# Optimization experiments

Measured on AMD Instinct MI355X. Metric: run time of the kernel, lower is better.

Reference implementation:

```python
import jax, jax.numpy as jnp
import numpy as np

B = 16          # graphs per batch
NN = 2000       # nodes per graph (num_nodes)
N = B * NN      # total nodes in the batched graph
F_IN = 128      # input node features
H, C = 4, 64    # heads, per-head out channels (both GAT layers)
HC = H * C
DEG = 12        # average degree per node
FC1, FC2, OUT = 512, 128, 1
FC_IN = 6 * NN  # len(which_layer) = 6


def setup_inputs() -> dict:
    key = jax.random.key(0)
    ks = jax.random.split(key, 32)

    def g(i, shape, s=0.05):
        return jax.random.normal(ks[i], shape, jnp.float32) * s

    # within-graph random edges, no self loops (GATConv removes then re-adds them)
    src_l = jax.random.randint(ks[0], (B, NN * DEG), 0, NN)
    off = jax.random.randint(ks[1], (B, NN * DEG), 1, NN)
    dst_l = (src_l + off) % NN
    goff = (jnp.arange(B) * NN)[:, None]
    edge_index = jnp.stack([(src_l + goff).reshape(-1),
                            (dst_l + goff).reshape(-1)]).astype(jnp.int32)

    return {
        "x": g(2, (N, F_IN), 1.0),
        "W1": g(3, (F_IN, HC)), "att_src1": g(4, (H, C)), "att_dst1": g(5, (H, C)),
        "b1": jnp.zeros((HC,), jnp.float32),
        "W2": g(6, (HC, HC)), "att_src2": g(7, (H, C)), "att_dst2": g(8, (H, C)),
        "b2": jnp.zeros((HC,), jnp.float32),
        "pw1": g(9, (HC, 1)), "pb1": jnp.zeros((1,), jnp.float32),
        "pw2": g(10, (HC, 1)), "pb2": jnp.zeros((1,), jnp.float32),
        "ln_w": jnp.ones((NN,), jnp.float32), "ln_b": jnp.zeros((NN,), jnp.float32),
        "sex_emb": g(11, (2, NN)), "mut_emb": g(12, (4, NN)),
        "age_w": g(13, (NN,)), "age_b": jnp.zeros((NN,), jnp.float32),
        "fw1": g(14, (FC_IN, FC1)), "fb1": jnp.zeros((FC1,), jnp.float32),
        "fw2": g(15, (FC1, FC2)), "fb2": jnp.zeros((FC2,), jnp.float32),
        "fw3": g(16, (FC2, OUT)), "fb3": jnp.zeros((OUT,), jnp.float32),
        "age": jax.random.uniform(ks[17], (B,), jnp.float32),
        "edge_index": edge_index,
        "sex": jax.random.randint(ks[18], (B,), 0, 2),
        "mutation": jax.random.randint(ks[19], (B,), 0, 4),
    }


def _layer_norm(x, w, b, eps=1e-5):
    mu = jnp.mean(x, -1, keepdims=True)
    var = jnp.mean((x - mu) ** 2, -1, keepdims=True)
    return (x - mu) / jnp.sqrt(var + eps) * w + b


def _gat_conv(x, W, att_src, att_dst, bias, src, dst):
    h = (x @ W).reshape(N, H, C)                         # [N,H,C]
    a_s = jnp.sum(h * att_src[None], -1)                 # [N,H]
    a_d = jnp.sum(h * att_dst[None], -1)                 # [N,H]
    alpha = jax.nn.leaky_relu(a_s[src] + a_d[dst], 0.2)  # [E,H]
    m = jax.ops.segment_max(alpha, dst, num_segments=N)  # segment softmax over dst
    e = jnp.exp(alpha - m[dst])
    denom = jax.ops.segment_sum(e, dst, num_segments=N)
    a = e / (denom[dst] + 1e-16)
    out = jax.ops.segment_sum(a[:, :, None] * h[src], dst, num_segments=N)
    return out.reshape(N, HC) + bias


def _forward(x, W1, att_src1, att_dst1, b1, W2, att_src2, att_dst2, b2,
             pw1, pb1, pw2, pb2, ln_w, ln_b, sex_emb, mut_emb, age_w, age_b,
             fw1, fb1, fw2, fb2, fw3, fb3, age, edge_index, sex, mutation):
    loop = jnp.arange(N, dtype=edge_index.dtype)         # self loops added by GATConv
    src = jnp.concatenate([edge_index[0], loop])
    dst = jnp.concatenate([edge_index[1], loop])

    x0 = jnp.mean(x, -1).reshape(B, NN)                  # to_dense_batch(mean(x,-1))

    h = jax.nn.relu(_gat_conv(x, W1, att_src1, att_dst1, b1, src, dst))
    x1 = (h @ pw1 + pb1).squeeze(-1).reshape(B, NN)
    h = jax.nn.relu(_gat_conv(h, W2, att_src2, att_dst2, b2, src, dst))
    x2 = (h @ pw2 + pb2).squeeze(-1).reshape(B, NN)

    x0 = _layer_norm(x0, ln_w, ln_b)
    x1 = _layer_norm(x1, ln_w, ln_b)
    x2 = _layer_norm(x2, ln_w, ln_b)
    ms = jnp.concatenate([x0, x1, x2], axis=1)           # [B, 3*NN]

    demo = jnp.concatenate([sex_emb[sex], mut_emb[mutation],
                            age[:, None] * age_w[None, :] + age_b], axis=1)
    t = jnp.concatenate([demo, ms], axis=1)              # [B, 6*NN]
    t = jax.nn.relu(t @ fw1 + fb1)
    t = jax.nn.relu(t @ fw2 + fb2)
    pred = t @ fw3 + fb3                                 # [B, 1]
    return pred, x0, x1, x2, ms


def reference(x, W1, att_src1, att_dst1, b1, W2, att_src2, att_dst2, b2,
              pw1, pb1, pw2, pb2, ln_w, ln_b, sex_emb, mut_emb, age_w, age_b,
              fw1, fb1, fw2, fb2, fw3, fb3, age, edge_index, sex, mutation):
    return _forward(x, W1, att_src1, att_dst1, b1, W2, att_src2, att_dst2, b2,
                    pw1, pb1, pw2, pb2, ln_w, ln_b, sex_emb, mut_emb, age_w, age_b,
                    fw1, fb1, fw2, fb2, fw3, fb3, age, edge_index, sex, mutation)
```

## Files before the change

### kernel.cpp

```cpp
#include <hip/hip_runtime.h>
#include <math.h>

#define NTOT   32000
#define NNODE  2000
#define NB     16
#define FIN    128
#define HCDIM  256
#define NH     4
#define FC1DIM 512
#define FC2DIM 128
#define FCIN   12000
#define KC1    50
#define NCH1   240
#define CAP    64
#define BK     32
#define LPITCH 40
#define TRB    384
#define DEMOB  375

typedef __attribute__((ext_vector_type(8))) short bf16x8;
typedef __attribute__((ext_vector_type(4))) float f32x4;

__device__ inline float4 ld4(const float* p){ return *reinterpret_cast<const float4*>(p); }
__device__ inline void st4(float* p, float4 v){ *reinterpret_cast<float4*>(p) = v; }
__device__ inline float4 add4(float4 a, float4 b){ return make_float4(a.x+b.x,a.y+b.y,a.z+b.z,a.w+b.w); }
__device__ inline float lrelu(float x){ return x > 0.f ? x : 0.2f*x; }
__device__ inline float4 leaky4(float4 a){ return make_float4(lrelu(a.x),lrelu(a.y),lrelu(a.z),lrelu(a.w)); }
__device__ inline float4 exp4u(float4 a){ return make_float4(__expf(a.x),__expf(a.y),__expf(a.z),__expf(a.w)); }
__device__ inline float dot4(float4 a, float4 b){ return a.x*b.x + a.y*b.y + a.z*b.z + a.w*b.w; }
__device__ inline float selh(float4 v, int h){ return h==0 ? v.x : (h==1 ? v.y : (h==2 ? v.z : v.w)); }

__device__ inline unsigned short f2bf(float f){
  unsigned int u = __float_as_uint(f);
  u += 0x7FFFu + ((u >> 16) & 1u);
  return (unsigned short)(u >> 16);
}
__device__ inline float bf2f(unsigned short h){
  return __uint_as_float(((unsigned int)h) << 16);
}
__device__ inline float4 ldbf4(const unsigned short* p){
  ushort4 v = *reinterpret_cast<const ushort4*>(p);
  return make_float4(bf2f(v.x), bf2f(v.y), bf2f(v.z), bf2f(v.w));
}

__global__ __launch_bounds__(256) void k_prep(const float* __restrict__ x,
                                              unsigned short* __restrict__ xb,
                                              float* __restrict__ x0r,
                                              int* __restrict__ cnt){
  int gid = blockIdx.x*256 + threadIdx.x;
  if(gid < NTOT) cnt[gid] = 0;
  int lane = threadIdx.x & 63, wv = threadIdx.x >> 6;
  int n = blockIdx.x*4 + wv;
  const float* r = x + (size_t)n*FIN;
  float2 v = *reinterpret_cast<const float2*>(r + lane*2);
  unsigned int packed = (unsigned int)f2bf(v.x) | ((unsigned int)f2bf(v.y) << 16);
  *reinterpret_cast<unsigned int*>(xb + (size_t)n*FIN + lane*2) = packed;
  float s = v.x + v.y;
  #pragma unroll
  for(int off=1; off<64; off<<=1) s += __shfl_xor(s, off);
  if(lane == 0) x0r[n] = s * (1.0f/FIN);
}

__global__ void k_misc(const int* __restrict__ src, const int* __restrict__ dst,
                       int* __restrict__ cnt, int* __restrict__ col, int e0, int eb,
                       const float* __restrict__ W1, const float* __restrict__ W2,
                       unsigned short* __restrict__ W1t, unsigned short* __restrict__ W2t,
                       const float* __restrict__ sexemb, const float* __restrict__ mutemb,
                       const float* __restrict__ agew, const float* __restrict__ ageb,
                       const float* __restrict__ age, const int* __restrict__ sex,
                       const int* __restrict__ mut, float* __restrict__ t){
  int blk = blockIdx.x;
  if(blk < eb){
    int i = blk*256 + threadIdx.x;
    if(i < e0){
      int d = dst[i];
      int slot = atomicAdd(&cnt[d], 1);
      if(slot < CAP) col[(d<<6) + slot] = src[i];
    }
  } else if(blk < eb + TRB){
    int idx = (blk - eb)*256 + threadIdx.x;
    if(idx < HCDIM*FIN){
      int n = idx / FIN, k = idx - n*FIN;
      W1t[idx] = f2bf(W1[(size_t)k*HCDIM + n]);
    } else {
      int j = idx - HCDIM*FIN;
      int n = j / HCDIM, k = j - n*HCDIM;
      W2t[j] = f2bf(W2[(size_t)k*HCDIM + n]);
    }
  } else {
    int i = (blk - eb - TRB)*256 + threadIdx.x;
    int b = i / (3*NNODE);
    int j = i - b*(3*NNODE);
    float v;
    if(j < NNODE)          v = sexemb[sex[b]*NNODE + j];
    else if(j < 2*NNODE)   v = mutemb[mut[b]*NNODE + (j - NNODE)];
    else                   v = age[b]*agew[j - 2*NNODE] + ageb[j - 2*NNODE];
    t[b*FCIN + j] = v;
  }
}

__global__ __launch_bounds__(256) void k_gemm_bf(const unsigned short* __restrict__ A,
                                                 const unsigned short* __restrict__ Bt,
                                                 unsigned short* __restrict__ C,
                                                 const float* __restrict__ attS,
                                                 const float* __restrict__ attD,
                                                 float* __restrict__ a_s,
                                                 float* __restrict__ a_d,
                                                 int M, int K){
  __shared__ unsigned short As[128][LPITCH];
  __shared__ unsigned short Bs[128][LPITCH];
  int tid = threadIdx.x;
  int lane = tid & 63, wv = tid >> 6;
  int wm = (wv & 1)*64, wn = (wv >> 1)*64;
  int m0 = blockIdx.y*128, n0 = blockIdx.x*128;
  int l15 = lane & 15, lq = lane >> 4;
  f32x4 acc[4][4];
  #pragma unroll
  for(int i=0;i<4;i++)
    #pragma unroll
    for(int j=0;j<4;j++)
      acc[i][j] = (f32x4){0.f,0.f,0.f,0.f};

  int r = tid >> 2, c = (tid & 3)*8;
  for(int k0 = 0; k0 < K; k0 += BK){
    *reinterpret_cast<uint4*>(&As[r][c])    = *reinterpret_cast<const uint4*>(A  + (size_t)(m0+r)*K + k0 + c);
    *reinterpret_cast<uint4*>(&As[r+64][c]) = *reinterpret_cast<const uint4*>(A  + (size_t)(m0+r+64)*K + k0 + c);
    *reinterpret_cast<uint4*>(&Bs[r][c])    = *reinterpret_cast<const uint4*>(Bt + (size_t)(n0+r)*K + k0 + c);
    *reinterpret_cast<uint4*>(&Bs[r+64][c]) = *reinterpret_cast<const uint4*>(Bt + (size_t)(n0+r+64)*K + k0 + c);
    __syncthreads();
    bf16x8 af[4], bfr[4];
    #pragma unroll
    for(int i=0;i<4;i++){
      af[i]  = *reinterpret_cast<const bf16x8*>(&As[wm + i*16 + l15][lq*8]);
      bfr[i] = *reinterpret_cast<const bf16x8*>(&Bs[wn + i*16 + l15][lq*8]);
    }
    #pragma unroll
    for(int mi=0;mi<4;mi++)
      #pragma unroll
      for(int ni=0;ni<4;ni++)
        acc[mi][ni] = __builtin_amdgcn_mfma_f32_16x16x32_bf16(af[mi], bfr[ni], acc[mi][ni], 0, 0, 0);
    __syncthreads();
  }
  #pragma unroll
  for(int mi=0;mi<4;mi++){
    #pragma unroll
    for(int ni=0;ni<4;ni++){
      int cn = n0 + wn + ni*16 + l15;
      #pragma unroll
      for(int rg=0;rg<4;rg++){
        int rm = m0 + wm + mi*16 + lq*4 + rg;
        C[(size_t)rm*HCDIM + cn] = f2bf(acc[mi][ni][rg]);
      }
    }
  }
  int head = (n0 + wn) >> 6;
  float avs[4], avd[4];
  #pragma unroll
  for(int ni=0;ni<4;ni++){
    int cc = ni*16 + l15;
    avs[ni] = attS[head*64 + cc];
    avd[ni] = attD[head*64 + cc];
  }
  #pragma unroll
  for(int mi=0;mi<4;mi++){
    #pragma unroll
    for(int rg=0;rg<4;rg++){
      float ps = 0.f, pd = 0.f;
      #pragma unroll
      for(int ni=0;ni<4;ni++){
        float v = acc[mi][ni][rg];
        ps = fmaf(avs[ni], v, ps);
        pd = fmaf(avd[ni], v, pd);
      }
      #pragma unroll
      for(int off=1; off<16; off<<=1){
        ps += __shfl_xor(ps, off);
        pd += __shfl_xor(pd, off);
      }
      if(l15 == 0){
        int rm = m0 + wm + mi*16 + lq*4 + rg;
        a_s[rm*4 + head] = ps;
        a_d[rm*4 + head] = pd;
      }
    }
  }
}

template<int STORE>
__global__ __launch_bounds__(256) void k_agg(const unsigned short* __restrict__ hpre,
                                             const float* __restrict__ a_s,
                                             const float* __restrict__ a_d,
                                             const int* __restrict__ cnt,
                                             const int* __restrict__ col,
                                             const float* __restrict__ bias,
                                             const float* __restrict__ pw,
                                             const float* __restrict__ pb,
                                             unsigned short* __restrict__ hout,
                                             float* __restrict__ xraw){
  __shared__ float4 ew[4][CAP];
  __shared__ int    cols[4][CAP];
  int tid = threadIdx.x;
  int lane = tid & 63, wv = tid >> 6;
  int blk  = blockIdx.x;
  int xcd  = blk & 7;
  int slot = blk >> 3;
  int half = slot / 500;
  int g    = xcd + 8*half;
  int n    = g*NNODE + (slot - half*500)*4 + wv;
  int f0 = lane*4;
  int hl = lane >> 4;
  float4 ad   = ld4(a_d + n*4);
  float4 asn  = ld4(a_s + n*4);
  float4 eself = exp4u(leaky4(add4(asn, ad)));
  int deg = min(cnt[n], CAP);
  int base = n << 6;
  if(lane < deg){
    int s = col[base + lane];
    cols[wv][lane] = s;
    ew[wv][lane] = exp4u(leaky4(add4(ld4(a_s + s*4), ad)));
  }
  float es = selh(eself, hl);
  float dsum = es;
  float4 hv = ldbf4(hpre + (size_t)n*HCDIM + f0);
  float4 acc = make_float4(es*hv.x, es*hv.y, es*hv.z, es*hv.w);
  const float* ewf = (const float*)&ew[wv][0];
  const int*   cwf = &cols[wv][0];
  for(int e = 0; e < deg; e++){
    int s = cwf[e];
    float w = ewf[e*4 + hl];
    dsum += w;
    float4 h2 = ldbf4(hpre + (size_t)s*HCDIM + f0);
    acc.x = fmaf(w, h2.x, acc.x); acc.y = fmaf(w, h2.y, acc.y);
    acc.z = fmaf(w, h2.z, acc.z); acc.w = fmaf(w, h2.w, acc.w);
  }
  float invh = 1.0f / (dsum + 1e-16f);
  float4 b4 = ld4(bias + f0);
  acc = make_float4(fmaxf(fmaf(acc.x,invh,b4.x),0.f), fmaxf(fmaf(acc.y,invh,b4.y),0.f),
                    fmaxf(fmaf(acc.z,invh,b4.z),0.f), fmaxf(fmaf(acc.w,invh,b4.w),0.f));
  if(STORE){
    ushort4 hb = make_ushort4(f2bf(acc.x), f2bf(acc.y), f2bf(acc.z), f2bf(acc.w));
    *reinterpret_cast<ushort4*>(hout + (size_t)n*HCDIM + f0) = hb;
  }
  float part = dot4(acc, ld4(pw + f0));
  #pragma unroll
  for(int off=1; off<64; off<<=1) part += __shfl_xor(part, off);
  if(lane == 0) xraw[n] = part + pb[0];
}

__global__ __launch_bounds__(256) void k_ln3(const float* __restrict__ xraw0,
                                             const float* __restrict__ lnw,
                                             const float* __restrict__ lnb,
                                             float* __restrict__ out,
                                             float* __restrict__ t){
  int blk = blockIdx.x;
  int b = blk & 15, which = blk >> 4;
  const float* src = xraw0 + which*NTOT + b*NNODE;
  __shared__ float red[8];
  int tid = threadIdx.x, lane = tid & 63, wv = tid >> 6;
  float s = 0.f, ss = 0.f;
  for(int i = tid; i < NNODE; i += 256){ float v = src[i]; s += v; ss += v*v; }
  #pragma unroll
  for(int off=1; off<64; off<<=1){ s += __shfl_xor(s, off); ss += __shfl_xor(ss, off); }
  if(lane == 0){ red[wv] = s; red[4+wv] = ss; }
  __syncthreads();
  s  = red[0]+red[1]+red[2]+red[3];
  ss = red[4]+red[5]+red[6]+red[7];
  float mu  = s * (1.0f/NNODE);
  float var = ss * (1.0f/NNODE) - mu*mu;
  float inv = 1.0f / sqrtf(var + 1e-5f);
  float* o1 = out + 16 + which*(NB*NNODE) + b*NNODE;
  float* o2 = out + 16 + 3*(NB*NNODE) + b*(3*NNODE) + which*NNODE;
  float* o3 = t + b*FCIN + 3*NNODE + which*NNODE;
  for(int i = tid; i < NNODE; i += 256){
    float v = (src[i]-mu)*inv*lnw[i] + lnb[i];
    o1[i] = v; o2[i] = v; o3[i] = v;
  }
}

__global__ __launch_bounds__(256) void k_fc1p(const float* __restrict__ t,
                                              const float* __restrict__ fw1,
                                              float* __restrict__ partial){
  __shared__ float ts[NB][KC1];
  __shared__ float red[NB][FC1DIM];
  int tid = threadIdx.x;
  int half = tid >> 7;
  int c4 = (tid & 127) * 4;
  int k0 = blockIdx.x * KC1;
  for(int i = tid; i < NB*KC1; i += 256){
    int b = i / KC1, kk = i - b*KC1;
    ts[b][kk] = t[b*FCIN + k0 + kk];
  }
  __syncthreads();
  float4 acc[NB];
  #pragma unroll
  for(int b=0;b<NB;b++) acc[b] = make_float4(0.f,0.f,0.f,0.f);
  for(int kk = half; kk < KC1; kk += 2){
    float4 w = ld4(fw1 + (size_t)(k0+kk)*FC1DIM + c4);
    #pragma unroll
    for(int b=0;b<NB;b++){
      float tv = ts[b][kk];
      acc[b].x = fmaf(tv, w.x, acc[b].x);
      acc[b].y = fmaf(tv, w.y, acc[b].y);
      acc[b].z = fmaf(tv, w.z, acc[b].z);
      acc[b].w = fmaf(tv, w.w, acc[b].w);
    }
  }
  if(half == 1){
    #pragma unroll
    for(int b=0;b<NB;b++) st4(&red[b][c4], acc[b]);
  }
  __syncthreads();
  if(half == 0){
    float* po = partial + (size_t)blockIdx.x*(NB*FC1DIM);
    #pragma unroll
    for(int b=0;b<NB;b++){
      float4 r = ld4(&red[b][c4]);
      st4(po + b*FC1DIM + c4, add4(acc[b], r));
    }
  }
}

__global__ void k_fc1r(const float* __restrict__ partial, const float* __restrict__ fb1,
                       float* __restrict__ t1){
  int i = blockIdx.x*blockDim.x + threadIdx.x;
  float s = fb1[i & (FC1DIM-1)];
  for(int c=0;c<NCH1;c++) s += partial[(size_t)c*(NB*FC1DIM) + i];
  t1[i] = fmaxf(s, 0.f);
}

__global__ __launch_bounds__(128) void k_head2(const float* __restrict__ t1,
                                               const float* __restrict__ fw2,
                                               const float* __restrict__ fb2,
                                               const float* __restrict__ fw3,
                                               const float* __restrict__ fb3,
                                               float* __restrict__ pred){
  __shared__ float red[2];
  int b = blockIdx.x, j = threadIdx.x;
  const float* tr = t1 + b*FC1DIM;
  float s = fb2[j];
  for(int k=0;k<FC1DIM;k++) s = fmaf(tr[k], fw2[k*FC2DIM+j], s);
  s = fmaxf(s, 0.f) * fw3[j];
  #pragma unroll
  for(int off=1; off<64; off<<=1) s += __shfl_xor(s, off);
  int lane = j & 63, wv = j >> 6;
  if(lane == 0) red[wv] = s;
  __syncthreads();
  if(j == 0) pred[b] = red[0] + red[1] + fb3[0];
}

extern "C" void kernel_launch(void* const* d_in, const int* in_sizes, int n_in,
                              void* d_out, int out_size, void* d_ws, size_t ws_size,
                              hipStream_t stream) {
  const float* x       = (const float*)d_in[0];
  const float* W1      = (const float*)d_in[1];
  const float* attS1   = (const float*)d_in[2];
  const float* attD1   = (const float*)d_in[3];
  const float* b1      = (const float*)d_in[4];
  const float* W2      = (const float*)d_in[5];
  const float* attS2   = (const float*)d_in[6];
  const float* attD2   = (const float*)d_in[7];
  const float* b2      = (const float*)d_in[8];
  const float* pw1     = (const float*)d_in[9];
  const float* pb1     = (const float*)d_in[10];
  const float* pw2     = (const float*)d_in[11];
  const float* pb2     = (const float*)d_in[12];
  const float* lnw     = (const float*)d_in[13];
  const float* lnb     = (const float*)d_in[14];
  const float* sexemb  = (const float*)d_in[15];
  const float* mutemb  = (const float*)d_in[16];
  const float* agew    = (const float*)d_in[17];
  const float* ageb    = (const float*)d_in[18];
  const float* fw1     = (const float*)d_in[19];
  const float* fb1     = (const float*)d_in[20];
  const float* fw2     = (const float*)d_in[21];
  const float* fb2     = (const float*)d_in[22];
  const float* fw3     = (const float*)d_in[23];
  const float* fb3     = (const float*)d_in[24];
  const float* age     = (const float*)d_in[25];
  const int*   eidx    = (const int*)d_in[26];
  const int*   sex     = (const int*)d_in[27];
  const int*   mut     = (const int*)d_in[28];
  const int E0 = in_sizes[26] / 2;
  const int* esrc = eidx;
  const int* edst = eidx + E0;

  float* out = (float*)d_out;

  float* w = (float*)d_ws;
  float* a_s  = w;
  float* a_d  = a_s + NTOT*NH;
  float* x0r  = a_d + NTOT*NH;
  float* x1r  = x0r + NTOT;
  float* x2r  = x1r + NTOT;
  float* tbuf = x2r + NTOT;
  float* part = tbuf + NB*FCIN;
  float* t1   = part + (size_t)NCH1*NB*FC1DIM;
  unsigned short* xb  = (unsigned short*)(t1 + NB*FC1DIM);
  unsigned short* hA  = xb  + (size_t)NTOT*FIN;
  unsigned short* hB  = hA  + (size_t)NTOT*HCDIM;
  unsigned short* W1t = hB  + (size_t)NTOT*HCDIM;
  unsigned short* W2t = W1t + HCDIM*FIN;
  int* cnt    = (int*)(W2t + HCDIM*HCDIM);
  int* col    = cnt + NTOT;
  (void)ws_size; (void)n_in; (void)out_size;

  const int eb = (E0 + 255)/256;

  k_prep<<<NTOT/4, 256, 0, stream>>>(x, xb, x0r, cnt);
  k_misc<<<eb + TRB + DEMOB, 256, 0, stream>>>(esrc, edst, cnt, col, E0, eb,
                                               W1, W2, W1t, W2t,
                                               sexemb, mutemb, agew, ageb,
                                               age, sex, mut, tbuf);

  k_gemm_bf<<<dim3(HCDIM/128, NTOT/128), 256, 0, stream>>>(xb, W1t, hA, attS1, attD1, a_s, a_d, NTOT, FIN);
  k_agg<1><<<NTOT/4, 256, 0, stream>>>(hA, a_s, a_d, cnt, col, b1, pw1, pb1, hB, x1r);

  k_gemm_bf<<<dim3(HCDIM/128, NTOT/128), 256, 0, stream>>>(hB, W2t, hA, attS2, attD2, a_s, a_d, NTOT, HCDIM);
  k_agg<0><<<NTOT/4, 256, 0, stream>>>(hA, a_s, a_d, cnt, col, b2, pw2, pb2, hB, x2r);

  k_ln3<<<3*NB, 256, 0, stream>>>(x0r, lnw, lnb, out, tbuf);

  k_fc1p<<<NCH1, 256, 0, stream>>>(tbuf, fw1, part);
  k_fc1r<<<(NB*FC1DIM)/256, 256, 0, stream>>>(part, fb1, t1);
  k_head2<<<NB, 128, 0, stream>>>(t1, fw2, fb2, fw3, fb3, out);
}
```

Baseline: 280.9 us.

## Fuse bf16 cast into GEMM, hide layernorms in agg kernels, split fc1 reduction

The first GEMM now reads x as fp32 and converts it to bf16 while staging tiles. This removes the separate bf16 copy of x and its round trip through memory. The x0 row mean moves into k_misc, and the x0 and x1 layernorms run as 16 extra blocks inside the following aggregation kernels, leaving only the x2 layernorm standalone. The fc1 partial reduction now splits its 240 chunks across four waves per output with a shared-memory combine, giving more parallel blocks. The costs are an extra zeroing launch, more fp32 global reads in GEMM1, and a little branching in the agg kernels.

```diff
diff --git a/kernel.cpp b/kernel.cpp
--- a/kernel.cpp
+++ b/kernel.cpp
@@ -35,6 +35,9 @@
   u += 0x7FFFu + ((u >> 16) & 1u);
   return (unsigned short)(u >> 16);
 }
+__device__ inline unsigned int pk2bf(float a, float b){
+  return (unsigned int)f2bf(a) | ((unsigned int)f2bf(b) << 16);
+}
 __device__ inline float bf2f(unsigned short h){
   return __uint_as_float(((unsigned int)h) << 16);
 }
@@ -43,22 +46,34 @@
   return make_float4(bf2f(v.x), bf2f(v.y), bf2f(v.z), bf2f(v.w));
 }
 
-__global__ __launch_bounds__(256) void k_prep(const float* __restrict__ x,
-                                              unsigned short* __restrict__ xb,
-                                              float* __restrict__ x0r,
-                                              int* __restrict__ cnt){
-  int gid = blockIdx.x*256 + threadIdx.x;
-  if(gid < NTOT) cnt[gid] = 0;
-  int lane = threadIdx.x & 63, wv = threadIdx.x >> 6;
-  int n = blockIdx.x*4 + wv;
-  const float* r = x + (size_t)n*FIN;
-  float2 v = *reinterpret_cast<const float2*>(r + lane*2);
-  unsigned int packed = (unsigned int)f2bf(v.x) | ((unsigned int)f2bf(v.y) << 16);
-  *reinterpret_cast<unsigned int*>(xb + (size_t)n*FIN + lane*2) = packed;
-  float s = v.x + v.y;
-  #pragma unroll
-  for(int off=1; off<64; off<<=1) s += __shfl_xor(s, off);
-  if(lane == 0) x0r[n] = s * (1.0f/FIN);
+__global__ __launch_bounds__(256) void k_zero(int* __restrict__ cnt){
+  int i = blockIdx.x*256 + threadIdx.x;
+  if(i < NTOT) cnt[i] = 0;
+}
+
+__device__ __forceinline__ void ln_impl(const float* __restrict__ src,
+                                        const float* __restrict__ lnw,
+                                        const float* __restrict__ lnb,
+                                        float* __restrict__ o1,
+                                        float* __restrict__ o2,
+                                        float* __restrict__ o3,
+                                        float* red){
+  int tid = threadIdx.x, lane = tid & 63, wv = tid >> 6;
+  float s = 0.f, ss = 0.f;
+  for(int i = tid; i < NNODE; i += 256){ float v = src[i]; s += v; ss += v*v; }
+  #pragma unroll
+  for(int off=1; off<64; off<<=1){ s += __shfl_xor(s, off); ss += __shfl_xor(ss, off); }
+  if(lane == 0){ red[wv] = s; red[4+wv] = ss; }
+  __syncthreads();
+  s  = red[0]+red[1]+red[2]+red[3];
+  ss = red[4]+red[5]+red[6]+red[7];
+  float mu  = s * (1.0f/NNODE);
+  float var = ss * (1.0f/NNODE) - mu*mu;
+  float inv = 1.0f / sqrtf(var + 1e-5f);
+  for(int i = tid; i < NNODE; i += 256){
+    float v = (src[i]-mu)*inv*lnw[i] + lnb[i];
+    o1[i] = v; o2[i] = v; o3[i] = v;
+  }
 }
 
 __global__ void k_misc(const int* __restrict__ src, const int* __restrict__ dst,
@@ -68,7 +83,8 @@
                        const float* __restrict__ sexemb, const float* __restrict__ mutemb,
                        const float* __restrict__ agew, const float* __restrict__ ageb,
                        const float* __restrict__ age, const int* __restrict__ sex,
-                       const int* __restrict__ mut, float* __restrict__ t){
+                       const int* __restrict__ mut, float* __restrict__ t,
+                       const float* __restrict__ x, float* __restrict__ x0r){
   int blk = blockIdx.x;
   if(blk < eb){
     int i = blk*256 + threadIdx.x;
@@ -87,7 +103,7 @@
       int n = j / HCDIM, k = j - n*HCDIM;
       W2t[j] = f2bf(W2[(size_t)k*HCDIM + n]);
     }
-  } else {
+  } else if(blk < eb + TRB + DEMOB){
     int i = (blk - eb - TRB)*256 + threadIdx.x;
     int b = i / (3*NNODE);
     int j = i - b*(3*NNODE);
@@ -96,10 +112,20 @@
     else if(j < 2*NNODE)   v = mutemb[mut[b]*NNODE + (j - NNODE)];
     else                   v = age[b]*agew[j - 2*NNODE] + ageb[j - 2*NNODE];
     t[b*FCIN + j] = v;
-  }
-}
-
-__global__ __launch_bounds__(256) void k_gemm_bf(const unsigned short* __restrict__ A,
+  } else {
+    int lane = threadIdx.x & 63, wv = threadIdx.x >> 6;
+    int n = (blk - eb - TRB - DEMOB)*4 + wv;
+    const float* r = x + (size_t)n*FIN;
+    float2 v = *reinterpret_cast<const float2*>(r + lane*2);
+    float s = v.x + v.y;
+    #pragma unroll
+    for(int off=1; off<64; off<<=1) s += __shfl_xor(s, off);
+    if(lane == 0) x0r[n] = s * (1.0f/FIN);
+  }
+}
+
+template<int AF32>
+__global__ __launch_bounds__(256) void k_gemm_bf(const void* __restrict__ Av,
                                                  const unsigned short* __restrict__ Bt,
                                                  unsigned short* __restrict__ C,
                                                  const float* __restrict__ attS,
@@ -107,6 +133,8 @@
                                                  float* __restrict__ a_s,
                                                  float* __restrict__ a_d,
                                                  int M, int K){
+  const unsigned short* A = (const unsigned short*)Av;
+  const float*         Af = (const float*)Av;
   __shared__ unsigned short As[128][LPITCH];
   __shared__ unsigned short Bs[128][LPITCH];
   int tid = threadIdx.x;
@@ -123,8 +151,22 @@
 
   int r = tid >> 2, c = (tid & 3)*8;
   for(int k0 = 0; k0 < K; k0 += BK){
-    *reinterpret_cast<uint4*>(&As[r][c])    = *reinterpret_cast<const uint4*>(A  + (size_t)(m0+r)*K + k0 + c);
-    *reinterpret_cast<uint4*>(&As[r+64][c]) = *reinterpret_cast<const uint4*>(A  + (size_t)(m0+r+64)*K + k0 + c);
+    if(AF32){
+      const float* pa  = Af + (size_t)(m0+r)*K + k0 + c;
+      const float* pa2 = Af + (size_t)(m0+r+64)*K + k0 + c;
+      float4 u0 = ld4(pa),  u1 = ld4(pa+4);
+      float4 v0 = ld4(pa2), v1 = ld4(pa2+4);
+      uint4 w0, w1;
+      w0.x = pk2bf(u0.x,u0.y); w0.y = pk2bf(u0.z,u0.w);
+      w0.z = pk2bf(u1.x,u1.y); w0.w = pk2bf(u1.z,u1.w);
+      w1.x = pk2bf(v0.x,v0.y); w1.y = pk2bf(v0.z,v0.w);
+      w1.z = pk2bf(v1.x,v1.y); w1.w = pk2bf(v1.z,v1.w);
+      *reinterpret_cast<uint4*>(&As[r][c])    = w0;
+      *reinterpret_cast<uint4*>(&As[r+64][c]) = w1;
+    } else {
+      *reinterpret_cast<uint4*>(&As[r][c])    = *reinterpret_cast<const uint4*>(A  + (size_t)(m0+r)*K + k0 + c);
+      *reinterpret_cast<uint4*>(&As[r+64][c]) = *reinterpret_cast<const uint4*>(A  + (size_t)(m0+r+64)*K + k0 + c);
+    }
     *reinterpret_cast<uint4*>(&Bs[r][c])    = *reinterpret_cast<const uint4*>(Bt + (size_t)(n0+r)*K + k0 + c);
     *reinterpret_cast<uint4*>(&Bs[r+64][c]) = *reinterpret_cast<const uint4*>(Bt + (size_t)(n0+r+64)*K + k0 + c);
     __syncthreads();
@@ -196,12 +238,28 @@
                                              const float* __restrict__ pw,
                                              const float* __restrict__ pb,
                                              unsigned short* __restrict__ hout,
-                                             float* __restrict__ xraw){
+                                             float* __restrict__ xraw,
+                                             const float* __restrict__ lnsrc,
+                                             const float* __restrict__ lnw,
+                                             const float* __restrict__ lnb,
+                                             float* __restrict__ out,
+                                             float* __restrict__ t,
+                                             int which){
   __shared__ float4 ew[4][CAP];
   __shared__ int    cols[4][CAP];
+  __shared__ float  lred[8];
+  int bx = blockIdx.x;
+  if(bx < 16){
+    int b = bx;
+    ln_impl(lnsrc + b*NNODE, lnw, lnb,
+            out + 16 + which*(NB*NNODE) + b*NNODE,
+            out + 16 + 3*(NB*NNODE) + b*(3*NNODE) + which*NNODE,
+            t + b*FCIN + 3*NNODE + which*NNODE, lred);
+    return;
+  }
   int tid = threadIdx.x;
   int lane = tid & 63, wv = tid >> 6;
-  int blk  = blockIdx.x;
+  int blk  = bx - 16;
   int xcd  = blk & 7;
   int slot = blk >> 3;
   int half = slot / 500;
@@ -247,34 +305,17 @@
   if(lane == 0) xraw[n] = part + pb[0];
 }
 
-__global__ __launch_bounds__(256) void k_ln3(const float* __restrict__ xraw0,
-                                             const float* __restrict__ lnw,
-                                             const float* __restrict__ lnb,
-                                             float* __restrict__ out,
-                                             float* __restrict__ t){
-  int blk = blockIdx.x;
-  int b = blk & 15, which = blk >> 4;
-  const float* src = xraw0 + which*NTOT + b*NNODE;
+__global__ __launch_bounds__(256) void k_lnx2(const float* __restrict__ x2r,
+                                              const float* __restrict__ lnw,
+                                              const float* __restrict__ lnb,
+                                              float* __restrict__ out,
+                                              float* __restrict__ t){
   __shared__ float red[8];
-  int tid = threadIdx.x, lane = tid & 63, wv = tid >> 6;
-  float s = 0.f, ss = 0.f;
-  for(int i = tid; i < NNODE; i += 256){ float v = src[i]; s += v; ss += v*v; }
-  #pragma unroll
-  for(int off=1; off<64; off<<=1){ s += __shfl_xor(s, off); ss += __shfl_xor(ss, off); }
-  if(lane == 0){ red[wv] = s; red[4+wv] = ss; }
-  __syncthreads();
-  s  = red[0]+red[1]+red[2]+red[3];
-  ss = red[4]+red[5]+red[6]+red[7];
-  float mu  = s * (1.0f/NNODE);
-  float var = ss * (1.0f/NNODE) - mu*mu;
-  float inv = 1.0f / sqrtf(var + 1e-5f);
-  float* o1 = out + 16 + which*(NB*NNODE) + b*NNODE;
-  float* o2 = out + 16 + 3*(NB*NNODE) + b*(3*NNODE) + which*NNODE;
-  float* o3 = t + b*FCIN + 3*NNODE + which*NNODE;
-  for(int i = tid; i < NNODE; i += 256){
-    float v = (src[i]-mu)*inv*lnw[i] + lnb[i];
-    o1[i] = v; o2[i] = v; o3[i] = v;
-  }
+  int b = blockIdx.x;
+  ln_impl(x2r + b*NNODE, lnw, lnb,
+          out + 16 + 2*(NB*NNODE) + b*NNODE,
+          out + 16 + 3*(NB*NNODE) + b*(3*NNODE) + 2*NNODE,
+          t + b*FCIN + 3*NNODE + 2*NNODE, red);
 }
 
 __global__ __launch_bounds__(256) void k_fc1p(const float* __restrict__ t,
@@ -320,12 +361,22 @@
   }
 }
 
-__global__ void k_fc1r(const float* __restrict__ partial, const float* __restrict__ fb1,
-                       float* __restrict__ t1){
-  int i = blockIdx.x*blockDim.x + threadIdx.x;
-  float s = fb1[i & (FC1DIM-1)];
-  for(int c=0;c<NCH1;c++) s += partial[(size_t)c*(NB*FC1DIM) + i];
-  t1[i] = fmaxf(s, 0.f);
+__global__ __launch_bounds__(256) void k_fc1r(const float* __restrict__ partial,
+                                              const float* __restrict__ fb1,
+                                              float* __restrict__ t1){
+  __shared__ float red[3][64];
+  int tid = threadIdx.x;
+  int e = blockIdx.x*64 + (tid & 63);
+  int g = tid >> 6;
+  float s = 0.f;
+  for(int c = g*60; c < g*60 + 60; c++) s += partial[(size_t)c*(NB*FC1DIM) + e];
+  if(g) red[g-1][tid & 63] = s;
+  __syncthreads();
+  if(g == 0){
+    s += red[0][tid & 63] + red[1][tid & 63] + red[2][tid & 63];
+    s += fb1[e & (FC1DIM-1)];
+    t1[e] = fmaxf(s, 0.f);
+  }
 }
 
 __global__ __launch_bounds__(128) void k_head2(const float* __restrict__ t1,
@@ -395,8 +446,7 @@
   float* tbuf = x2r + NTOT;
   float* part = tbuf + NB*FCIN;
   float* t1   = part + (size_t)NCH1*NB*FC1DIM;
-  unsigned short* xb  = (unsigned short*)(t1 + NB*FC1DIM);
-  unsigned short* hA  = xb  + (size_t)NTOT*FIN;
+  unsigned short* hA  = (unsigned short*)(t1 + NB*FC1DIM);
   unsigned short* hB  = hA  + (size_t)NTOT*HCDIM;
   unsigned short* W1t = hB  + (size_t)NTOT*HCDIM;
   unsigned short* W2t = W1t + HCDIM*FIN;
@@ -406,21 +456,23 @@
 
   const int eb = (E0 + 255)/256;
 
-  k_prep<<<NTOT/4, 256, 0, stream>>>(x, xb, x0r, cnt);
-  k_misc<<<eb + TRB + DEMOB, 256, 0, stream>>>(esrc, edst, cnt, col, E0, eb,
+  k_zero<<<(NTOT+255)/256, 256, 0, stream>>>(cnt);
+  k_misc<<<eb + TRB + DEMOB + NTOT/4, 256, 0, stream>>>(esrc, edst, cnt, col, E0, eb,
                                                W1, W2, W1t, W2t,
                                                sexemb, mutemb, agew, ageb,
-                                               age, sex, mut, tbuf);
-
-  k_gemm_bf<<<dim3(HCDIM/128, NTOT/128), 256, 0, stream>>>(xb, W1t, hA, attS1, attD1, a_s, a_d, NTOT, FIN);
-  k_agg<1><<<NTOT/4, 256, 0, stream>>>(hA, a_s, a_d, cnt, col, b1, pw1, pb1, hB, x1r);
-
-  k_gemm_bf<<<dim3(HCDIM/128, NTOT/128), 256, 0, stream>>>(hB, W2t, hA, attS2, attD2, a_s, a_d, NTOT, HCDIM);
-  k_agg<0><<<NTOT/4, 256, 0, stream>>>(hA, a_s, a_d, cnt, col, b2, pw2, pb2, hB, x2r);
-
-  k_ln3<<<3*NB, 256, 0, stream>>>(x0r, lnw, lnb, out, tbuf);
+                                               age, sex, mut, tbuf, x, x0r);
+
+  k_gemm_bf<1><<<dim3(HCDIM/128, NTOT/128), 256, 0, stream>>>(x, W1t, hA, attS1, attD1, a_s, a_d, NTOT, FIN);
+  k_agg<1><<<16 + NTOT/4, 256, 0, stream>>>(hA, a_s, a_d, cnt, col, b1, pw1, pb1, hB, x1r,
+                                            x0r, lnw, lnb, out, tbuf, 0);
+
+  k_gemm_bf<0><<<dim3(HCDIM/128, NTOT/128), 256, 0, stream>>>(hB, W2t, hA, attS2, attD2, a_s, a_d, NTOT, HCDIM);
+  k_agg<0><<<16 + NTOT/4, 256, 0, stream>>>(hA, a_s, a_d, cnt, col, b2, pw2, pb2, hB, x2r,
+                                            x1r, lnw, lnb, out, tbuf, 1);
+
+  k_lnx2<<<NB, 256, 0, stream>>>(x2r, lnw, lnb, out, tbuf);
 
   k_fc1p<<<NCH1, 256, 0, stream>>>(tbuf, fw1, part);
-  k_fc1r<<<(NB*FC1DIM)/256, 256, 0, stream>>>(part, fb1, t1);
+  k_fc1r<<<(NB*FC1DIM)/64, 256, 0, stream>>>(part, fb1, t1);
   k_head2<<<NB, 128, 0, stream>>>(t1, fw2, fb2, fw3, fb3, out);
 }
```

New measurement: 267.7 us. 4.7% less time.
